# Optimization experiments

Measured on AMD Instinct MI355X. Metric: run time of the kernel, lower is better.

The kernel has to match this reference:

```python
import jax, jax.numpy as jnp
import numpy as np

EPS = 1e-3

def layer_norm(x, w, b):
    mu = jnp.mean(x, axis=-1, keepdims=True)
    var = jnp.var(x, axis=-1, keepdims=True)
    return (x - mu) * jax.lax.rsqrt(var + EPS) * w + b

def setup_inputs() -> dict:
    key = jax.random.key(0)
    B, T, C, H = 8, 1024, 1024, 16
    Dh, F = C // H, 4 * C
    ks = jax.random.split(key, 12)
    s = 0.02
    return {
        "x":  jax.random.normal(ks[0], (B, T, C), jnp.float32),
        "Wq": jax.random.normal(ks[1], (H, C, Dh), jnp.float32) * s,
        "bq": jnp.zeros((H, Dh), jnp.float32),
        "Wk": jax.random.normal(ks[2], (H, C, Dh), jnp.float32) * s,
        "bk": jnp.zeros((H, Dh), jnp.float32),
        "Wv": jax.random.normal(ks[3], (H, C, Dh), jnp.float32) * s,
        "bv": jnp.zeros((H, Dh), jnp.float32),
        "Wp": jax.random.normal(ks[4], (C, C), jnp.float32) * s,
        "bp": jnp.zeros((C,), jnp.float32),
        "W1": jax.random.normal(ks[5], (C, F), jnp.float32) * s,
        "b1": jnp.zeros((F,), jnp.float32),
        "W2": jax.random.normal(ks[6], (F, C), jnp.float32) * s,
        "b2": jnp.zeros((C,), jnp.float32),
        "ln1_w": jnp.ones((C,), jnp.float32),
        "ln1_b": jnp.zeros((C,), jnp.float32),
        "ln2_w": jnp.ones((C,), jnp.float32),
        "ln2_b": jnp.zeros((C,), jnp.float32),
    }

def reference(x, Wq, bq, Wk, bk, Wv, bv, Wp, bp, W1, b1, W2, b2, ln1_w, ln1_b, ln2_w, ln2_b):
    B, T, C = x.shape
    # x = ln1(x); x = x + mha(x)   (residual taken from post-LN x, as in source)
    x1 = layer_norm(x, ln1_w, ln1_b)
    # all heads vectorized: q/k/v are [B, H, T, Dh]
    q = jnp.einsum('btc,hcd->bhtd', x1, Wq) + bq[:, None, :]
    k = jnp.einsum('btc,hcd->bhtd', x1, Wk) + bk[:, None, :]
    v = jnp.einsum('btc,hcd->bhtd', x1, Wv) + bv[:, None, :]
    # NOTE: source scales by full embed dim C (not head_size), and multiplies
    # the UN-softmaxed scores `wei` by v (softmax result is discarded).
    wei = jnp.einsum('bhtd,bhsd->bhts', q, k) * (C ** -0.5)
    heads = jnp.einsum('bhts,bhsd->bhtd', wei, v)            # [B,H,T,Dh]
    cat = heads.transpose(0, 2, 1, 3).reshape(B, T, C)        # concat heads
    attn = cat @ Wp + bp
    x2 = layer_norm(x1 + attn, ln2_w, ln2_b)
    h = jax.nn.gelu(x2 @ W1 + b1, approximate=False)
    return x2 + (h @ W2 + b2)
```

## Files before the change

### kernel.cpp

```cpp
#include <hip/hip_runtime.h>

typedef unsigned short u16;
typedef unsigned int u32;
typedef unsigned long long u64;
typedef __attribute__((ext_vector_type(8))) short bf16x8;
typedef __attribute__((ext_vector_type(4))) float f32x4;

__device__ __forceinline__ float b2f(u16 v) {
  union { u32 u; float f; } c; c.u = ((u32)v) << 16; return c.f;
}
__device__ __forceinline__ u16 f2b(float f) {
  union { float f; u32 u; } c; c.f = f;
  return (u16)((c.u + 0x7fffu + ((c.u >> 16) & 1u)) >> 16);
}

__device__ __forceinline__ void g2l16(const u16* g, u16* l) {
  __builtin_amdgcn_global_load_lds(
      (const __attribute__((address_space(1))) u32*)g,
      (__attribute__((address_space(3))) u32*)l,
      16, 0, 0);
}

__device__ __forceinline__ float gelu_fast(float x) {
  float z2 = -1.5957691216057308f * x * (1.0f + 0.044715f * x * x);
  z2 = fminf(fmaxf(z2, -30.f), 30.f);
  float t = __expf(z2);
  return x * __builtin_amdgcn_rcpf(1.0f + t);
}

__global__ __launch_bounds__(256)
void repack_qkv_tiled(const float* __restrict__ Wq, const float* __restrict__ Wk,
                      const float* __restrict__ Wv, u16* __restrict__ WT) {
  __shared__ u16 tile[64][65];
  const int sh = blockIdx.y, sel = sh >> 4, h = sh & 15;
  const float* W = (sel == 0) ? Wq : ((sel == 1) ? Wk : Wv);
  const int k0 = blockIdx.x * 64;
  {
    const int d = threadIdx.x & 63, r = threadIdx.x >> 6;
    #pragma unroll
    for (int i = 0; i < 16; ++i) {
      int k = r * 16 + i;
      tile[k][d] = f2b(W[(size_t)h * 65536 + (size_t)(k0 + k) * 64 + d]);
    }
  }
  __syncthreads();
  {
    const int k = threadIdx.x & 63, dd = threadIdx.x >> 6;
    #pragma unroll
    for (int i = 0; i < 16; ++i) {
      int d2 = dd * 16 + i;
      WT[((size_t)sel * 1024 + h * 64 + d2) * 1024 + k0 + k] = tile[k][d2];
    }
  }
}

__global__ __launch_bounds__(256)
void transpose_tiled(const float* __restrict__ W, u16* __restrict__ WT,
                     int N, int K) {
  __shared__ u16 tile[32][33];
  const int bx = blockIdx.x * 32;
  const int by = blockIdx.y * 32;
  const int tx = threadIdx.x & 31, ty = threadIdx.x >> 5;
  #pragma unroll
  for (int i = 0; i < 4; ++i) {
    int k = ty + i * 8;
    tile[k][tx] = f2b(W[(size_t)(by + k) * N + bx + tx]);
  }
  __syncthreads();
  #pragma unroll
  for (int i = 0; i < 4; ++i) {
    int n = ty + i * 8;
    WT[(size_t)(bx + n) * K + by + tx] = tile[tx][n];
  }
}

__global__ __launch_bounds__(256)
void ln_f32_kernel(const float* __restrict__ X, const float* __restrict__ G,
                   const float* __restrict__ Bt, u16* __restrict__ O) {
  const int row = blockIdx.x;
  const int tid = threadIdx.x;
  const float* xr = X + (size_t)row * 1024;
  float4 xv = *(const float4*)(xr + tid * 4);
  float v0 = xv.x, v1 = xv.y, v2 = xv.z, v3 = xv.w;
  float s = v0 + v1 + v2 + v3;
  float q = v0 * v0 + v1 * v1 + v2 * v2 + v3 * v3;
  #pragma unroll
  for (int off = 32; off > 0; off >>= 1) {
    s += __shfl_down(s, off);
    q += __shfl_down(q, off);
  }
  __shared__ float red[8];
  int wave = tid >> 6, lane = tid & 63;
  if (lane == 0) { red[wave] = s; red[4 + wave] = q; }
  __syncthreads();
  s = red[0] + red[1] + red[2] + red[3];
  q = red[4] + red[5] + red[6] + red[7];
  float mean = s * (1.f / 1024.f);
  float var = q * (1.f / 1024.f) - mean * mean;
  float rstd = rsqrtf(var + 1e-3f);
  float4 gv = *(const float4*)(G + tid * 4);
  float4 bv = *(const float4*)(Bt + tid * 4);
  ushort4 ov;
  ov.x = f2b((v0 - mean) * rstd * gv.x + bv.x);
  ov.y = f2b((v1 - mean) * rstd * gv.y + bv.y);
  ov.z = f2b((v2 - mean) * rstd * gv.z + bv.z);
  ov.w = f2b((v3 - mean) * rstd * gv.w + bv.w);
  *(ushort4*)(O + (size_t)row * 1024 + tid * 4) = ov;
}

__global__ __launch_bounds__(256)
void ln_bf16_kernel(const u16* __restrict__ X, const float* __restrict__ G,
                    const float* __restrict__ Bt, u16* __restrict__ O) {
  const int row = blockIdx.x;
  const int tid = threadIdx.x;
  const u16* xr = X + (size_t)row * 1024;
  ushort4 xv = *(const ushort4*)(xr + tid * 4);
  float v0 = b2f(xv.x), v1 = b2f(xv.y), v2 = b2f(xv.z), v3 = b2f(xv.w);
  float s = v0 + v1 + v2 + v3;
  float q = v0 * v0 + v1 * v1 + v2 * v2 + v3 * v3;
  #pragma unroll
  for (int off = 32; off > 0; off >>= 1) {
    s += __shfl_down(s, off);
    q += __shfl_down(q, off);
  }
  __shared__ float red[8];
  int wave = tid >> 6, lane = tid & 63;
  if (lane == 0) { red[wave] = s; red[4 + wave] = q; }
  __syncthreads();
  s = red[0] + red[1] + red[2] + red[3];
  q = red[4] + red[5] + red[6] + red[7];
  float mean = s * (1.f / 1024.f);
  float var = q * (1.f / 1024.f) - mean * mean;
  float rstd = rsqrtf(var + 1e-3f);
  float4 gv = *(const float4*)(G + tid * 4);
  float4 bv = *(const float4*)(Bt + tid * 4);
  ushort4 ov;
  ov.x = f2b((v0 - mean) * rstd * gv.x + bv.x);
  ov.y = f2b((v1 - mean) * rstd * gv.y + bv.y);
  ov.z = f2b((v2 - mean) * rstd * gv.z + bv.z);
  ov.w = f2b((v3 - mean) * rstd * gv.w + bv.w);
  *(ushort4*)(O + (size_t)row * 1024 + tid * 4) = ov;
}

template <int EPI>
__global__ __launch_bounds__(256)
void gemm_nt(const u16* __restrict__ A, const u16* __restrict__ BT,
             void* __restrict__ Cout,
             const float* __restrict__ bias0, const float* __restrict__ bias1,
             const float* __restrict__ bias2, const u16* __restrict__ resid,
             int M, int N, int K) {
  __shared__ __align__(16) u16 smem[32768];
  const int tid = threadIdx.x;
  const int m0 = blockIdx.y * 128;
  const int n0 = blockIdx.x * 128;
  const int wave = tid >> 6, lane = tid & 63;
  const int wm = wave & 1, wn = wave >> 1;
  const int quad = lane >> 4, l16 = lane & 15;

  f32x4 acc[4][4];
  #pragma unroll
  for (int i = 0; i < 4; ++i)
    #pragma unroll
    for (int j = 0; j < 4; ++j) acc[i][j] = (f32x4){0.f, 0.f, 0.f, 0.f};

  const int rowS = tid >> 3;
  const int swz = ((tid & 7) ^ ((tid >> 3) & 7)) * 8;
  const u16* aB = A + (size_t)(m0 + rowS) * K + swz;
  const u16* bB = BT + (size_t)(n0 + rowS) * K + swz;
  const size_t rstep = (size_t)32 * K;

  const int nt = K >> 6;

  auto stage = [&](int p, int kt) {
    u16* aD = &smem[(u32)p * 8192 + (u32)tid * 8];
    u16* bD = &smem[16384u + (u32)p * 8192 + (u32)tid * 8];
    const int k0 = kt * 64;
    #pragma unroll
    for (int cc = 0; cc < 4; ++cc) {
      g2l16(aB + k0 + cc * rstep, aD + cc * 2048);
      g2l16(bB + k0 + cc * rstep, bD + cc * 2048);
    }
  };

  stage(0, 0);

  for (int t = 0; t < nt; ++t) {
    const int p = t & 1;
    asm volatile("s_waitcnt vmcnt(0)" ::: "memory");
    __builtin_amdgcn_s_barrier();
    const u16* As = &smem[(u32)p * 8192];
    const u16* Bs = &smem[16384u + (u32)p * 8192];

    bf16x8 aF[2][4], bF[2][4];
    #pragma unroll
    for (int ks = 0; ks < 2; ++ks) {
      const int sOff = (((ks * 4 + quad) ^ (l16 & 7)) * 8);
      #pragma unroll
      for (int i = 0; i < 4; ++i)
        aF[ks][i] = *(const bf16x8*)&As[(wm * 64 + i * 16 + l16) * 64 + sOff];
      #pragma unroll
      for (int j = 0; j < 4; ++j)
        bF[ks][j] = *(const bf16x8*)&Bs[(wn * 64 + j * 16 + l16) * 64 + sOff];
    }
    if (t + 1 < nt) stage(p ^ 1, t + 1);
    #pragma unroll
    for (int ks = 0; ks < 2; ++ks)
      #pragma unroll
      for (int i = 0; i < 4; ++i)
        #pragma unroll
        for (int j = 0; j < 4; ++j)
          acc[i][j] = __builtin_amdgcn_mfma_f32_16x16x32_bf16(
              aF[ks][i], bF[ks][j], acc[i][j], 0, 0, 0);
  }
  __syncthreads();

  #pragma unroll
  for (int half = 0; half < 2; ++half) {
    if (wm == half) {
      #pragma unroll
      for (int i = 0; i < 4; ++i) {
        const int fsw = (i * 4 + quad) & 7;
        #pragma unroll
        for (int j = 0; j < 4; ++j) {
          const int chunk = (wn * 8 + j * 2 + (l16 >> 3)) ^ fsw;
          const int base = chunk * 8 + (l16 & 7);
          #pragma unroll
          for (int rr = 0; rr < 4; ++rr) {
            const int lrow = i * 16 + quad * 4 + rr;
            smem[lrow * 128 + base] = f2b(acc[i][j][rr]);
          }
        }
      }
    }
    __syncthreads();
    #pragma unroll
    for (int s = 0; s < 4; ++s) {
      const int lrow = s * 16 + (tid >> 4);
      const int chunk = tid & 15;
      const int fsw = (lrow >> 2) & 7;
      bf16x8 cv = *(const bf16x8*)&smem[lrow * 128 + ((chunk ^ fsw) * 8)];
      const int gr = m0 + half * 64 + lrow;
      const int gc = n0 + chunk * 8;
      const float* bp_ = bias0;
      int cb = gc;
      if (EPI == 0) {
        const int selb = gc >> 10;
        bp_ = (selb == 0) ? bias0 : ((selb == 1) ? bias1 : bias2);
        cb = gc & 1023;
      }
      float4 bv0 = *(const float4*)(bp_ + cb);
      float4 bv1 = *(const float4*)(bp_ + cb + 4);
      float vv[8];
      #pragma unroll
      for (int e = 0; e < 8; ++e) {
        float be = (e < 4) ? ((const float*)&bv0)[e] : ((const float*)&bv1)[e - 4];
        vv[e] = b2f(((const u16*)&cv)[e]) + be;
      }
      if (EPI == 2) {
        #pragma unroll
        for (int e = 0; e < 8; ++e) vv[e] = gelu_fast(vv[e]);
      }
      if (EPI == 1 || EPI == 3) {
        bf16x8 rv = *(const bf16x8*)(resid + (size_t)gr * N + gc);
        #pragma unroll
        for (int e = 0; e < 8; ++e) vv[e] += b2f(((const u16*)&rv)[e]);
      }
      if (EPI == 3) {
        float4 o0 = {vv[0], vv[1], vv[2], vv[3]};
        float4 o1 = {vv[4], vv[5], vv[6], vv[7]};
        float* op = (float*)Cout + (size_t)gr * N + gc;
        *(float4*)op = o0;
        *(float4*)(op + 4) = o1;
      } else {
        bf16x8 ov;
        #pragma unroll
        for (int e = 0; e < 8; ++e) ((u16*)&ov)[e] = f2b(vv[e]);
        *(bf16x8*)((u16*)Cout + (size_t)gr * N + gc) = ov;
      }
    }
    __syncthreads();
  }
}

__global__ __launch_bounds__(256)
void attn_m_kernel(const u16* __restrict__ qkv, float* __restrict__ Mbuf) {
  const int bh = blockIdx.x;
  const int half = blockIdx.y;
  const int b = bh >> 4, h = bh & 15;
  const u16* Kp = qkv + (size_t)b * 1024 * 3072 + 1024 + h * 64;
  const u16* Vp = Kp + 1024 + half * 32;
  __shared__ __align__(16) float Ks[64 * 64];
  __shared__ __align__(16) float Vs[64 * 36];
  const int tid = threadIdx.x;
  const int d1 = tid & 63, d2b = (tid >> 6) * 8;
  const int lr = tid >> 3, lc = (tid & 7) * 8;
  const int vr = tid >> 2, vc = (tid & 3) * 8;
  float acc[8];
  #pragma unroll
  for (int j = 0; j < 8; ++j) acc[j] = 0.f;
  for (int t0 = 0; t0 < 1024; t0 += 64) {
    __syncthreads();
    #pragma unroll
    for (int it = 0; it < 2; ++it) {
      int r = it * 32 + lr;
      const u16* ks = Kp + (size_t)(t0 + r) * 3072 + lc;
      ushort4 a0 = *(const ushort4*)ks;
      ushort4 a1 = *(const ushort4*)(ks + 4);
      float* kd = &Ks[r * 64 + lc];
      kd[0] = b2f(a0.x); kd[1] = b2f(a0.y); kd[2] = b2f(a0.z); kd[3] = b2f(a0.w);
      kd[4] = b2f(a1.x); kd[5] = b2f(a1.y); kd[6] = b2f(a1.z); kd[7] = b2f(a1.w);
    }
    {
      const u16* vs = Vp + (size_t)(t0 + vr) * 3072 + vc;
      ushort4 c0 = *(const ushort4*)vs;
      ushort4 c1 = *(const ushort4*)(vs + 4);
      float* vd = &Vs[vr * 36 + vc];
      vd[0] = b2f(c0.x); vd[1] = b2f(c0.y); vd[2] = b2f(c0.z); vd[3] = b2f(c0.w);
      vd[4] = b2f(c1.x); vd[5] = b2f(c1.y); vd[6] = b2f(c1.z); vd[7] = b2f(c1.w);
    }
    __syncthreads();
    #pragma unroll 8
    for (int tt = 0; tt < 64; ++tt) {
      float kv = Ks[tt * 64 + d1];
      #pragma unroll
      for (int j = 0; j < 8; ++j) acc[j] += kv * Vs[tt * 36 + d2b + j];
    }
  }
  float* Mo = Mbuf + (size_t)bh * 4096 + d1 * 64 + half * 32 + d2b;
  #pragma unroll
  for (int j = 0; j < 8; ++j) Mo[j] = acc[j] * 0.03125f;
}

__global__ __launch_bounds__(256)
void attn_h_kernel(const u16* __restrict__ qkv, const float* __restrict__ Mbuf,
                   u16* __restrict__ cat) {
  const int bh = blockIdx.x;
  const int tch = blockIdx.y;
  const int b = bh >> 4, h = bh & 15;
  __shared__ __align__(16) float Ms[64 * 64];
  __shared__ __align__(16) float Qs[64 * 65];
  const int tid = threadIdx.x;
  const float* Msrc = Mbuf + (size_t)bh * 4096;
  #pragma unroll
  for (int i = 0; i < 16; ++i) Ms[i * 256 + tid] = Msrc[i * 256 + tid];
  const u16* Qp = qkv + (size_t)(b * 1024 + tch * 64) * 3072 + h * 64;
  {
    const int lr = tid >> 3, lc = (tid & 7) * 8;
    #pragma unroll
    for (int it = 0; it < 2; ++it) {
      int r = it * 32 + lr;
      const u16* qs = Qp + (size_t)r * 3072 + lc;
      ushort4 a0 = *(const ushort4*)qs;
      ushort4 a1 = *(const ushort4*)(qs + 4);
      float* qd = &Qs[r * 65 + lc];
      qd[0] = b2f(a0.x); qd[1] = b2f(a0.y); qd[2] = b2f(a0.z); qd[3] = b2f(a0.w);
      qd[4] = b2f(a1.x); qd[5] = b2f(a1.y); qd[6] = b2f(a1.z); qd[7] = b2f(a1.w);
    }
  }
  __syncthreads();
  const int tl = tid >> 2, db = (tid & 3) * 16;
  float acc[16];
  #pragma unroll
  for (int j = 0; j < 16; ++j) acc[j] = 0.f;
  #pragma unroll 4
  for (int k = 0; k < 64; ++k) {
    float qv = Qs[tl * 65 + k];
    #pragma unroll
    for (int j = 0; j < 16; ++j) acc[j] += qv * Ms[k * 64 + db + j];
  }
  u16* Cp = cat + (size_t)(b * 1024 + tch * 64 + tl) * 1024 + h * 64 + db;
  ushort4 o0 = {f2b(acc[0]), f2b(acc[1]), f2b(acc[2]), f2b(acc[3])};
  ushort4 o1 = {f2b(acc[4]), f2b(acc[5]), f2b(acc[6]), f2b(acc[7])};
  ushort4 o2 = {f2b(acc[8]), f2b(acc[9]), f2b(acc[10]), f2b(acc[11])};
  ushort4 o3 = {f2b(acc[12]), f2b(acc[13]), f2b(acc[14]), f2b(acc[15])};
  *(ushort4*)(Cp + 0) = o0;
  *(ushort4*)(Cp + 4) = o1;
  *(ushort4*)(Cp + 8) = o2;
  *(ushort4*)(Cp + 12) = o3;
}

extern "C" void kernel_launch(void* const* d_in, const int* in_sizes, int n_in,
                              void* d_out, int out_size, void* d_ws, size_t ws_size,
                              hipStream_t stream) {
  (void)in_sizes; (void)n_in; (void)out_size; (void)ws_size;
  const float* x     = (const float*)d_in[0];
  const float* Wq    = (const float*)d_in[1];
  const float* bq    = (const float*)d_in[2];
  const float* Wk    = (const float*)d_in[3];
  const float* bk    = (const float*)d_in[4];
  const float* Wv    = (const float*)d_in[5];
  const float* bv    = (const float*)d_in[6];
  const float* Wp    = (const float*)d_in[7];
  const float* bp    = (const float*)d_in[8];
  const float* W1    = (const float*)d_in[9];
  const float* b1    = (const float*)d_in[10];
  const float* W2    = (const float*)d_in[11];
  const float* b2    = (const float*)d_in[12];
  const float* ln1w  = (const float*)d_in[13];
  const float* ln1b  = (const float*)d_in[14];
  const float* ln2w  = (const float*)d_in[15];
  const float* ln2b  = (const float*)d_in[16];

  char* ws = (char*)d_ws;
  u16* x1    = (u16*)(ws);
  u16* qkv   = (u16*)(ws + 16777216);
  u16* cat   = (u16*)(ws + 67108864);
  u16* yb    = (u16*)(ws + 83886080);
  u16* x2    = (u16*)(ws + 100663296);
  u16* WqkvT = (u16*)(ws + 117440512);
  u16* WpT   = (u16*)(ws + 123731968);
  u16* W1T   = (u16*)(ws + 125829120);
  u16* W2T   = (u16*)(ws + 134217728);
  float* Mb  = (float*)(ws + 142606336);
  u16* hb    = (u16*)(ws + 16777216);

  repack_qkv_tiled<<<dim3(16, 48), 256, 0, stream>>>(Wq, Wk, Wv, WqkvT);
  transpose_tiled<<<dim3(32, 32), 256, 0, stream>>>(Wp, WpT, 1024, 1024);
  transpose_tiled<<<dim3(128, 32), 256, 0, stream>>>(W1, W1T, 4096, 1024);
  transpose_tiled<<<dim3(32, 128), 256, 0, stream>>>(W2, W2T, 1024, 4096);

  ln_f32_kernel<<<8192, 256, 0, stream>>>(x, ln1w, ln1b, x1);

  gemm_nt<0><<<dim3(24, 64), 256, 0, stream>>>(x1, WqkvT, qkv, bq, bk, bv, nullptr,
                                               8192, 3072, 1024);
  attn_m_kernel<<<dim3(128, 2), 256, 0, stream>>>(qkv, Mb);
  attn_h_kernel<<<dim3(128, 16), 256, 0, stream>>>(qkv, Mb, cat);

  gemm_nt<1><<<dim3(8, 64), 256, 0, stream>>>(cat, WpT, yb, bp, nullptr, nullptr, x1,
                                              8192, 1024, 1024);
  ln_bf16_kernel<<<8192, 256, 0, stream>>>(yb, ln2w, ln2b, x2);

  gemm_nt<2><<<dim3(32, 64), 256, 0, stream>>>(x2, W1T, hb, b1, nullptr, nullptr, nullptr,
                                               8192, 4096, 1024);
  gemm_nt<3><<<dim3(8, 64), 256, 0, stream>>>(hb, W2T, d_out, b2, nullptr, nullptr, x2,
                                              8192, 1024, 4096);
}
```

Baseline: 523.4 us.

## Halve GEMM K-tile with new LDS swizzle and vectorize attention LDS reads

```diff
diff --git a/kernel.cpp b/kernel.cpp
--- a/kernel.cpp
+++ b/kernel.cpp
@@ -149,7 +149,7 @@
              const float* __restrict__ bias0, const float* __restrict__ bias1,
              const float* __restrict__ bias2, const u16* __restrict__ resid,
              int M, int N, int K) {
-  __shared__ __align__(16) u16 smem[32768];
+  __shared__ __align__(16) u16 smem[16384];
   const int tid = threadIdx.x;
   const int m0 = blockIdx.y * 128;
   const int n0 = blockIdx.x * 128;
@@ -163,54 +163,49 @@
     #pragma unroll
     for (int j = 0; j < 4; ++j) acc[i][j] = (f32x4){0.f, 0.f, 0.f, 0.f};
 
-  const int rowS = tid >> 3;
-  const int swz = ((tid & 7) ^ ((tid >> 3) & 7)) * 8;
-  const u16* aB = A + (size_t)(m0 + rowS) * K + swz;
-  const u16* bB = BT + (size_t)(n0 + rowS) * K + swz;
-  const size_t rstep = (size_t)32 * K;
-
-  const int nt = K >> 6;
-
-  auto stage = [&](int p, int kt) {
-    u16* aD = &smem[(u32)p * 8192 + (u32)tid * 8];
-    u16* bD = &smem[16384u + (u32)p * 8192 + (u32)tid * 8];
-    const int k0 = kt * 64;
-    #pragma unroll
-    for (int cc = 0; cc < 4; ++cc) {
-      g2l16(aB + k0 + cc * rstep, aD + cc * 2048);
-      g2l16(bB + k0 + cc * rstep, bD + cc * 2048);
-    }
+  const int s7 = tid & 7, t8 = tid >> 3;
+  const int rS = 2 * t8 + (s7 & 1);
+  const int cS = ((s7 >> 1) ^ (t8 & 3)) * 8;
+  const u16* aS0 = A + (size_t)(m0 + rS) * K + cS;
+  const u16* aS1 = aS0 + (size_t)64 * K;
+  const u16* bS0 = BT + (size_t)(n0 + rS) * K + cS;
+  const u16* bS1 = bS0 + (size_t)64 * K;
+  u16* aD = &smem[(u32)tid * 8];
+  u16* bD = &smem[8192u + (u32)tid * 8];
+
+  auto stage = [&](int p, int koff) {
+    g2l16(aS0 + koff, aD + p * 4096);
+    g2l16(aS1 + koff, aD + p * 4096 + 2048);
+    g2l16(bS0 + koff, bD + p * 4096);
+    g2l16(bS1 + koff, bD + p * 4096 + 2048);
   };
 
+  const int g = l16 >> 1, par = l16 & 1;
+  const u32 slotq = (u32)(2 * (quad ^ (g & 3)) + par) * 8;
+  const u32 aBase = (u32)(wm * 32 + g) * 64 + slotq;
+  const u32 bBase = 8192u + (u32)(wn * 32 + g) * 64 + slotq;
+
+  const int nt = K >> 5;
   stage(0, 0);
 
   for (int t = 0; t < nt; ++t) {
     const int p = t & 1;
     asm volatile("s_waitcnt vmcnt(0)" ::: "memory");
     __builtin_amdgcn_s_barrier();
-    const u16* As = &smem[(u32)p * 8192];
-    const u16* Bs = &smem[16384u + (u32)p * 8192];
-
-    bf16x8 aF[2][4], bF[2][4];
-    #pragma unroll
-    for (int ks = 0; ks < 2; ++ks) {
-      const int sOff = (((ks * 4 + quad) ^ (l16 & 7)) * 8);
-      #pragma unroll
-      for (int i = 0; i < 4; ++i)
-        aF[ks][i] = *(const bf16x8*)&As[(wm * 64 + i * 16 + l16) * 64 + sOff];
+    if (t + 1 < nt) stage(p ^ 1, (t + 1) * 32);
+    const u16* pA = &smem[aBase + (u32)p * 4096];
+    const u16* pB = &smem[bBase + (u32)p * 4096];
+    bf16x8 aF[4], bF[4];
+    #pragma unroll
+    for (int i = 0; i < 4; ++i) aF[i] = *(const bf16x8*)(pA + i * 512);
+    #pragma unroll
+    for (int j = 0; j < 4; ++j) bF[j] = *(const bf16x8*)(pB + j * 512);
+    #pragma unroll
+    for (int i = 0; i < 4; ++i)
       #pragma unroll
       for (int j = 0; j < 4; ++j)
-        bF[ks][j] = *(const bf16x8*)&Bs[(wn * 64 + j * 16 + l16) * 64 + sOff];
-    }
-    if (t + 1 < nt) stage(p ^ 1, t + 1);
-    #pragma unroll
-    for (int ks = 0; ks < 2; ++ks)
-      #pragma unroll
-      for (int i = 0; i < 4; ++i)
-        #pragma unroll
-        for (int j = 0; j < 4; ++j)
-          acc[i][j] = __builtin_amdgcn_mfma_f32_16x16x32_bf16(
-              aF[ks][i], bF[ks][j], acc[i][j], 0, 0, 0);
+        acc[i][j] = __builtin_amdgcn_mfma_f32_16x16x32_bf16(
+            aF[i], bF[j], acc[i][j], 0, 0, 0);
   }
   __syncthreads();
 
@@ -292,12 +287,14 @@
   __shared__ __align__(16) float Ks[64 * 64];
   __shared__ __align__(16) float Vs[64 * 36];
   const int tid = threadIdx.x;
-  const int d1 = tid & 63, d2b = (tid >> 6) * 8;
+  const int d1p = (tid & 31) * 2, d2q = (tid >> 5) * 4;
   const int lr = tid >> 3, lc = (tid & 7) * 8;
   const int vr = tid >> 2, vc = (tid & 3) * 8;
-  float acc[8];
-  #pragma unroll
-  for (int j = 0; j < 8; ++j) acc[j] = 0.f;
+  float acc[2][4];
+  #pragma unroll
+  for (int a = 0; a < 2; ++a)
+    #pragma unroll
+    for (int j = 0; j < 4; ++j) acc[a][j] = 0.f;
   for (int t0 = 0; t0 < 1024; t0 += 64) {
     __syncthreads();
     #pragma unroll
@@ -321,14 +318,21 @@
     __syncthreads();
     #pragma unroll 8
     for (int tt = 0; tt < 64; ++tt) {
-      float kv = Ks[tt * 64 + d1];
+      float2 kv = *(const float2*)&Ks[tt * 64 + d1p];
+      float4 vv = *(const float4*)&Vs[tt * 36 + d2q];
       #pragma unroll
-      for (int j = 0; j < 8; ++j) acc[j] += kv * Vs[tt * 36 + d2b + j];
-    }
-  }
-  float* Mo = Mbuf + (size_t)bh * 4096 + d1 * 64 + half * 32 + d2b;
-  #pragma unroll
-  for (int j = 0; j < 8; ++j) Mo[j] = acc[j] * 0.03125f;
+      for (int j = 0; j < 4; ++j) {
+        acc[0][j] += kv.x * ((const float*)&vv)[j];
+        acc[1][j] += kv.y * ((const float*)&vv)[j];
+      }
+    }
+  }
+  #pragma unroll
+  for (int a = 0; a < 2; ++a) {
+    float4 o = {acc[a][0] * 0.03125f, acc[a][1] * 0.03125f,
+                acc[a][2] * 0.03125f, acc[a][3] * 0.03125f};
+    *(float4*)(Mbuf + (size_t)bh * 4096 + (d1p + a) * 64 + half * 32 + d2q) = o;
+  }
 }
 
 __global__ __launch_bounds__(256)
@@ -366,7 +370,11 @@
   for (int k = 0; k < 64; ++k) {
     float qv = Qs[tl * 65 + k];
     #pragma unroll
-    for (int j = 0; j < 16; ++j) acc[j] += qv * Ms[k * 64 + db + j];
+    for (int m4 = 0; m4 < 4; ++m4) {
+      float4 mv = *(const float4*)&Ms[k * 64 + db + m4 * 4];
+      #pragma unroll
+      for (int j = 0; j < 4; ++j) acc[m4 * 4 + j] += qv * ((const float*)&mv)[j];
+    }
   }
   u16* Cp = cat + (size_t)(b * 1024 + tch * 64 + tl) * 1024 + h * 64 + db;
   ushort4 o0 = {f2b(acc[0]), f2b(acc[1]), f2b(acc[2]), f2b(acc[3])};
```

New measurement: 510.5 us. 1.03x faster.

## Remap GEMM tiles per XCD for L2 locality; vectorize attention LDS reads

Applied to the files above, without the earlier changes.

```diff
diff --git a/kernel.cpp b/kernel.cpp
--- a/kernel.cpp
+++ b/kernel.cpp
@@ -148,11 +148,17 @@
              void* __restrict__ Cout,
              const float* __restrict__ bias0, const float* __restrict__ bias1,
              const float* __restrict__ bias2, const u16* __restrict__ resid,
-             int M, int N, int K) {
+             int M, int N, int K, int RA, int RB, int NRn) {
   __shared__ __align__(16) u16 smem[32768];
   const int tid = threadIdx.x;
-  const int m0 = blockIdx.y * 128;
-  const int n0 = blockIdx.x * 128;
+
+  const int xcd = blockIdx.x & 7;
+  const int s_ = blockIdx.x >> 3;
+  const int rm = xcd / NRn, rn = xcd - rm * NRn;
+  const int lm = s_ / RB, ln = s_ - lm * RB;
+  const int m0 = (rm * RA + lm) * 128;
+  const int n0 = (rn * RB + ln) * 128;
+
   const int wave = tid >> 6, lane = tid & 63;
   const int wm = wave & 1, wn = wave >> 1;
   const int quad = lane >> 4, l16 = lane & 15;
@@ -285,19 +291,19 @@
 __global__ __launch_bounds__(256)
 void attn_m_kernel(const u16* __restrict__ qkv, float* __restrict__ Mbuf) {
   const int bh = blockIdx.x;
-  const int half = blockIdx.y;
+  const int qtr = blockIdx.y;
   const int b = bh >> 4, h = bh & 15;
   const u16* Kp = qkv + (size_t)b * 1024 * 3072 + 1024 + h * 64;
-  const u16* Vp = Kp + 1024 + half * 32;
+  const u16* Vp = Kp + 1024 + qtr * 16;
   __shared__ __align__(16) float Ks[64 * 64];
-  __shared__ __align__(16) float Vs[64 * 36];
+  __shared__ __align__(16) float Vs[64 * 20];
   const int tid = threadIdx.x;
-  const int d1 = tid & 63, d2b = (tid >> 6) * 8;
+  const int d1 = tid & 63, d2q = (tid >> 6) * 4;
   const int lr = tid >> 3, lc = (tid & 7) * 8;
-  const int vr = tid >> 2, vc = (tid & 3) * 8;
-  float acc[8];
-  #pragma unroll
-  for (int j = 0; j < 8; ++j) acc[j] = 0.f;
+  const int vr = tid >> 2, vc = (tid & 3) * 4;
+  float acc[4];
+  #pragma unroll
+  for (int j = 0; j < 4; ++j) acc[j] = 0.f;
   for (int t0 = 0; t0 < 1024; t0 += 64) {
     __syncthreads();
     #pragma unroll
@@ -313,22 +319,21 @@
     {
       const u16* vs = Vp + (size_t)(t0 + vr) * 3072 + vc;
       ushort4 c0 = *(const ushort4*)vs;
-      ushort4 c1 = *(const ushort4*)(vs + 4);
-      float* vd = &Vs[vr * 36 + vc];
-      vd[0] = b2f(c0.x); vd[1] = b2f(c0.y); vd[2] = b2f(c0.z); vd[3] = b2f(c0.w);
-      vd[4] = b2f(c1.x); vd[5] = b2f(c1.y); vd[6] = b2f(c1.z); vd[7] = b2f(c1.w);
+      float4 vvw = {b2f(c0.x), b2f(c0.y), b2f(c0.z), b2f(c0.w)};
+      *(float4*)&Vs[vr * 20 + vc] = vvw;
     }
     __syncthreads();
     #pragma unroll 8
     for (int tt = 0; tt < 64; ++tt) {
       float kv = Ks[tt * 64 + d1];
-      #pragma unroll
-      for (int j = 0; j < 8; ++j) acc[j] += kv * Vs[tt * 36 + d2b + j];
-    }
-  }
-  float* Mo = Mbuf + (size_t)bh * 4096 + d1 * 64 + half * 32 + d2b;
-  #pragma unroll
-  for (int j = 0; j < 8; ++j) Mo[j] = acc[j] * 0.03125f;
+      float4 vv = *(const float4*)&Vs[tt * 20 + d2q];
+      #pragma unroll
+      for (int j = 0; j < 4; ++j) acc[j] += kv * ((const float*)&vv)[j];
+    }
+  }
+  float4 o = {acc[0] * 0.03125f, acc[1] * 0.03125f,
+              acc[2] * 0.03125f, acc[3] * 0.03125f};
+  *(float4*)(Mbuf + (size_t)bh * 4096 + d1 * 64 + qtr * 16 + d2q) = o;
 }
 
 __global__ __launch_bounds__(256)
@@ -366,7 +371,11 @@
   for (int k = 0; k < 64; ++k) {
     float qv = Qs[tl * 65 + k];
     #pragma unroll
-    for (int j = 0; j < 16; ++j) acc[j] += qv * Ms[k * 64 + db + j];
+    for (int m4 = 0; m4 < 4; ++m4) {
+      float4 mv = *(const float4*)&Ms[k * 64 + db + m4 * 4];
+      #pragma unroll
+      for (int j = 0; j < 4; ++j) acc[m4 * 4 + j] += qv * ((const float*)&mv)[j];
+    }
   }
   u16* Cp = cat + (size_t)(b * 1024 + tch * 64 + tl) * 1024 + h * 64 + db;
   ushort4 o0 = {f2b(acc[0]), f2b(acc[1]), f2b(acc[2]), f2b(acc[3])};
@@ -421,17 +430,17 @@
 
   ln_f32_kernel<<<8192, 256, 0, stream>>>(x, ln1w, ln1b, x1);
 
-  gemm_nt<0><<<dim3(24, 64), 256, 0, stream>>>(x1, WqkvT, qkv, bq, bk, bv, nullptr,
-                                               8192, 3072, 1024);
-  attn_m_kernel<<<dim3(128, 2), 256, 0, stream>>>(qkv, Mb);
+  gemm_nt<0><<<1536, 256, 0, stream>>>(x1, WqkvT, qkv, bq, bk, bv, nullptr,
+                                       8192, 3072, 1024, 16, 12, 2);
+  attn_m_kernel<<<dim3(128, 4), 256, 0, stream>>>(qkv, Mb);
   attn_h_kernel<<<dim3(128, 16), 256, 0, stream>>>(qkv, Mb, cat);
 
-  gemm_nt<1><<<dim3(8, 64), 256, 0, stream>>>(cat, WpT, yb, bp, nullptr, nullptr, x1,
-                                              8192, 1024, 1024);
+  gemm_nt<1><<<512, 256, 0, stream>>>(cat, WpT, yb, bp, nullptr, nullptr, x1,
+                                      8192, 1024, 1024, 8, 8, 1);
   ln_bf16_kernel<<<8192, 256, 0, stream>>>(yb, ln2w, ln2b, x2);
 
-  gemm_nt<2><<<dim3(32, 64), 256, 0, stream>>>(x2, W1T, hb, b1, nullptr, nullptr, nullptr,
-                                               8192, 4096, 1024);
-  gemm_nt<3><<<dim3(8, 64), 256, 0, stream>>>(hb, W2T, d_out, b2, nullptr, nullptr, x2,
-                                              8192, 1024, 4096);
-}
+  gemm_nt<2><<<2048, 256, 0, stream>>>(x2, W1T, hb, b1, nullptr, nullptr, nullptr,
+                                       8192, 4096, 1024, 16, 16, 2);
+  gemm_nt<3><<<512, 256, 0, stream>>>(hb, W2T, d_out, b2, nullptr, nullptr, x2,
+                                      8192, 1024, 4096, 8, 8, 1);
+}
```

Result: faster. 458.7 us (-12.4%).
